# Optimization experiments

Measured on AMD Instinct MI355X. Metric: run time of the kernel, lower is better.

## Reference

```python
import jax, jax.numpy as jnp
import numpy as np

B, S, D, H = 2, 2048, 1024, 16
DK = D // H


def setup_inputs() -> dict:
    key = jax.random.key(0)
    ks = jax.random.split(key, 12)
    s = 0.02
    inp = {
        "query": jax.random.normal(ks[0], (B, S, D), jnp.float32),
        "key": jax.random.normal(ks[1], (B, S, D), jnp.float32),
        "value": jax.random.normal(ks[2], (B, S, D), jnp.float32),
        # causal mask, broadcast over heads inside reference
        "mask": jnp.broadcast_to(jnp.tril(jnp.ones((S, S), jnp.int32)), (B, S, S)),
        "Wq": jax.random.normal(ks[3], (D, D), jnp.float32) * s,
        "bq": jnp.zeros((D,), jnp.float32),
        "Wk": jax.random.normal(ks[4], (D, D), jnp.float32) * s,
        "bk": jnp.zeros((D,), jnp.float32),
        "Wv": jax.random.normal(ks[5], (D, D), jnp.float32) * s,
        "bv": jnp.zeros((D,), jnp.float32),
        "Wo": jax.random.normal(ks[6], (D, D), jnp.float32) * s,
        "bo": jnp.zeros((D,), jnp.float32),
    }
    return inp


def reference(query, key, value, mask, Wq, bq, Wk, bk, Wv, bv, Wo, bo):
    b, sq, d = query.shape
    sk = key.shape[1]
    # projections (torch Linear: x @ W.T + b)
    q = (jnp.einsum('bsd,ed->bse', query, Wq) + bq).reshape(b, sq, H, DK).transpose(0, 2, 1, 3)
    k = (jnp.einsum('bsd,ed->bse', key, Wk) + bk).reshape(b, sk, H, DK).transpose(0, 2, 1, 3)
    v = (jnp.einsum('bsd,ed->bse', value, Wv) + bv).reshape(b, sk, H, DK).transpose(0, 2, 1, 3)
    # scaled dot-product attention, full score matrix as in the original
    scores = jnp.einsum('bhqd,bhkd->bhqk', q, k) / jnp.sqrt(jnp.float32(DK))
    scores = jnp.where(mask[:, None, :, :] == 0, jnp.float32(-1e9), scores)
    p_attn = jax.nn.softmax(scores, axis=-1)  # dropout omitted (eval mode)
    x = jnp.einsum('bhqk,bhkd->bhqd', p_attn, v)
    x = x.transpose(0, 2, 1, 3).reshape(b, sq, d)
    return jnp.einsum('bsd,ed->bse', x, Wo) + bo
```

## Files before the change

### kernel.cpp

```cpp
#include <hip/hip_runtime.h>
#include <hip/hip_bf16.h>

typedef __attribute__((ext_vector_type(8))) short short8;
typedef __attribute__((ext_vector_type(4))) short short4v;
typedef __attribute__((ext_vector_type(4))) float f32x4;

__device__ __forceinline__ short f2bf(float x) {
    __hip_bfloat16 h = __float2bfloat16(x);
    return __builtin_bit_cast(short, h);
}

__device__ __forceinline__ float exp2v(float x) {
    float r;
    asm("v_exp_f32 %0, %1" : "=v"(r) : "v"(x));
    return r;
}

__device__ __forceinline__ void gload16(const void* g, void* l) {
    __builtin_amdgcn_global_load_lds(
        (const __attribute__((address_space(1))) void*)g,
        (__attribute__((address_space(3))) void*)l, 16, 0, 0);
}

__global__ __launch_bounds__(256) void cvt_all_kernel(
    const float* __restrict__ q, const float* __restrict__ k,
    const float* __restrict__ v, const float* __restrict__ wq,
    const float* __restrict__ wk, const float* __restrict__ wv,
    const float* __restrict__ wo, short* __restrict__ dst) {
    size_t i = ((size_t)blockIdx.x * 256 + threadIdx.x) * 8;
    const float* s; size_t si;
    if (i < 12582912) {
        int w = (int)(i >> 22);
        s = (w == 0) ? q : (w == 1) ? k : v;
        si = i & 4194303;
    } else {
        size_t j = i - 12582912;
        int w = (int)(j >> 20);
        s = (w == 0) ? wq : (w == 1) ? wk : (w == 2) ? wv : wo;
        si = j & 1048575;
    }
    float4 a = *(const float4*)(s + si);
    float4 b = *(const float4*)(s + si + 4);
    short8 o;
    o[0] = f2bf(a.x); o[1] = f2bf(a.y); o[2] = f2bf(a.z); o[3] = f2bf(a.w);
    o[4] = f2bf(b.x); o[5] = f2bf(b.y); o[6] = f2bf(b.z); o[7] = f2bf(b.w);
    *(short8*)(dst + i) = o;
}

__device__ __forceinline__ void gemm128_core(const char* Ab, const char* Wb,
                                             short* Al, short* Bl,
                                             f32x4 (&acc)[4][4]) {
    const int tid = threadIdx.x, lane = tid & 63, wid = tid >> 6;
    const int lr = lane & 15, lg = lane >> 4;
    const int wr = wid >> 1, wc = wid & 1;
    for (int kt = 0; kt < 32; ++kt) {
#pragma unroll
        for (int i = 0; i < 2; ++i) {
            int slot0 = (wid * 2 + i) * 64;
            int slot = slot0 + lane;
            int row = slot >> 2;
            int cb = (slot & 3) << 4;
            size_t goff = (size_t)row * 2048 + (kt << 6) + cb;
            gload16(Ab + goff, (char*)Al + (slot0 << 4));
            gload16(Wb + goff, (char*)Bl + (slot0 << 4));
        }
        __syncthreads();
        short8 af[4], bw[4];
#pragma unroll
        for (int m = 0; m < 4; ++m)
            af[m] = *(const short8*)(Al + ((64 * wr + 16 * m + lr) << 5) + (lg << 3));
#pragma unroll
        for (int n = 0; n < 4; ++n)
            bw[n] = *(const short8*)(Bl + ((64 * wc + 16 * n + lr) << 5) + (lg << 3));
#pragma unroll
        for (int m = 0; m < 4; ++m)
#pragma unroll
            for (int n = 0; n < 4; ++n)
                acc[m][n] = __builtin_amdgcn_mfma_f32_16x16x32_bf16(
                    af[m], bw[n], acc[m][n], 0, 0, 0);
        __syncthreads();
    }
}

__global__ __launch_bounds__(256) void proj_gemm_kernel(
    const __hip_bfloat16* __restrict__ ins,
    const __hip_bfloat16* __restrict__ wts,
    const float* __restrict__ b0, const float* __restrict__ b1,
    const float* __restrict__ b2,
    __hip_bfloat16* __restrict__ outs) {
    __shared__ __align__(16) short Sh[2][128 * 32];
    const int lin = blockIdx.x;
    const int logical = ((lin & 7) * 96) + (lin >> 3);
    const int bx = logical & 7;
    const int by = (logical >> 3) & 31;
    const int z  = logical >> 8;
    const char* Ab = (const char*)(ins + (size_t)z * 4194304)
                     + (size_t)by * 128 * 2048;
    const char* Wb = (const char*)(wts + (size_t)z * 1048576)
                     + (size_t)bx * 128 * 2048;
    const float* bias = (z == 0) ? b0 : (z == 1) ? b1 : b2;
    __hip_bfloat16* out = outs + (size_t)z * 4194304;

    f32x4 acc[4][4] = {};
    gemm128_core(Ab, Wb, Sh[0], Sh[1], acc);

    const int tid = threadIdx.x, lane = tid & 63, wid = tid >> 6;
    const int lr = lane & 15, lg = lane >> 4;
    const int wr = wid >> 1, wc = wid & 1;
    int col0 = (bx << 7) + (wc << 6);
    int row0 = (by << 7) + (wr << 6);

    if (z == 2) {
        char* tb = (char*)Sh;
#pragma unroll
        for (int hm = 0; hm < 2; ++hm) {
            if (wr == hm) {
#pragma unroll
                for (int n = 0; n < 4; ++n) {
                    int coll = (wc << 6) + 16 * n + lr;
                    float bb = bias[(bx << 7) + coll];
#pragma unroll
                    for (int m = 0; m < 4; ++m) {
                        short4v vv;
#pragma unroll
                        for (int r = 0; r < 4; ++r)
                            vv[r] = f2bf(acc[m][n][r] + bb);
                        int byteoff = coll * 128 + 32 * m + 8 * lg;
                        *(short4v*)(tb + (byteoff ^ ((coll & 7) << 4))) = vv;
                    }
                }
            }
            __syncthreads();
#pragma unroll
            for (int i = 0; i < 4; ++i) {
                int c = tid + (i << 8);
                int row = c >> 3;
                int pos = c & 7;
                int lb = row * 128 + (pos << 4);
                short8 vv = *(const short8*)(tb + (lb ^ ((row & 7) << 4)));
                int e = (bx << 7) + row;
                int hh = e >> 6, dk = e & 63;
                int srow = (by << 7) + (hm << 6) + (pos << 3);
                int bat = srow >> 11, s = srow & 2047;
                *(short8*)((short*)out +
                    ((size_t)((bat * 16 + hh) * 64 + dk) << 11) + s) = vv;
            }
            __syncthreads();
        }
        return;
    }

    const float scale = (z == 0) ? 0.125f * 1.44269504f : 1.0f;
#pragma unroll
    for (int n = 0; n < 4; ++n) {
        int col = col0 + 16 * n + lr;
        float bb = bias[col];
        int hh = col >> 6, dk = col & 63;
#pragma unroll
        for (int m = 0; m < 4; ++m)
#pragma unroll
            for (int r = 0; r < 4; ++r) {
                int row = row0 + 16 * m + 4 * lg + r;
                int bat = row >> 11, s = row & 2047;
                out[((size_t)((bat * 16 + hh) * 2048 + s) << 6) + dk] =
                    __float2bfloat16((acc[m][n][r] + bb) * scale);
            }
    }
}

__global__ __launch_bounds__(256) void out_gemm_kernel(
    const __hip_bfloat16* __restrict__ X, const __hip_bfloat16* __restrict__ Wo,
    const float* __restrict__ bias, float* __restrict__ out) {
    __shared__ __align__(16) short Al[64 * 32];
    __shared__ __align__(16) short Bl[128 * 32];
    const int lin = blockIdx.x;
    const int logical = ((lin & 7) * 64) + (lin >> 3);
    const int bx = logical & 7;
    const int by = logical >> 3;
    const char* Ab = (const char*)X + (size_t)by * 64 * 2048;
    const char* Wb = (const char*)Wo + (size_t)bx * 128 * 2048;
    const int tid = threadIdx.x, lane = tid & 63, wid = tid >> 6;
    const int lr = lane & 15, lg = lane >> 4;

    f32x4 acc[4][2] = {};
    for (int kt = 0; kt < 32; ++kt) {
        {
            int slotA = (wid << 6) + lane;
            int rowA = slotA >> 2, cbA = (slotA & 3) << 4;
            gload16(Ab + (size_t)rowA * 2048 + (kt << 6) + cbA,
                    (char*)Al + (wid << 10));
#pragma unroll
            for (int i = 0; i < 2; ++i) {
                int slot0 = (wid * 2 + i) * 64;
                int slot = slot0 + lane;
                int rowB = slot >> 2, cbB = (slot & 3) << 4;
                gload16(Wb + (size_t)rowB * 2048 + (kt << 6) + cbB,
                        (char*)Bl + (slot0 << 4));
            }
        }
        __syncthreads();
        short8 af[4], bw[2];
#pragma unroll
        for (int m = 0; m < 4; ++m)
            af[m] = *(const short8*)(Al + ((16 * m + lr) << 5) + (lg << 3));
#pragma unroll
        for (int n = 0; n < 2; ++n)
            bw[n] = *(const short8*)(Bl + ((32 * wid + 16 * n + lr) << 5) + (lg << 3));
#pragma unroll
        for (int m = 0; m < 4; ++m)
#pragma unroll
            for (int n = 0; n < 2; ++n)
                acc[m][n] = __builtin_amdgcn_mfma_f32_16x16x32_bf16(
                    af[m], bw[n], acc[m][n], 0, 0, 0);
        __syncthreads();
    }

    int col0 = (bx << 7) + (wid << 5);
    int row0 = (by << 6);
#pragma unroll
    for (int n = 0; n < 2; ++n) {
        int col = col0 + 16 * n + lr;
        float bb = bias[col];
#pragma unroll
        for (int m = 0; m < 4; ++m)
#pragma unroll
            for (int r = 0; r < 4; ++r) {
                int row = row0 + 16 * m + 4 * lg + r;
                out[((size_t)row << 10) + col] = acc[m][n][r] + bb;
            }
    }
}

#define SWZB(row, cb) ((cb) ^ (((row) & 7) << 4))
#define RESCALE_THR 10.0f

__device__ __forceinline__ void stage_kv(const short* kg, const short* vtg,
                                         short* Kbuf, short* Vbuf, int kv0,
                                         int wid, int lane) {
#pragma unroll
    for (int i = 0; i < 2; ++i) {
        int slot0 = (wid * 2 + i) * 64;
        int slot = slot0 + lane;
        int row = slot >> 3;
        int cb = (slot & 7) << 4;
        const char* gk = (const char*)(kg + (size_t)(kv0 + row) * 64)
                         + SWZB(row, cb);
        gload16(gk, (char*)Kbuf + (slot0 << 4));
        const char* gv = (const char*)(vtg + (size_t)row * 2048 + kv0)
                         + SWZB(row, cb);
        gload16(gv, (char*)Vbuf + (slot0 << 4));
    }
}

__global__ __launch_bounds__(256) void attn_kernel(
    const __hip_bfloat16* __restrict__ qb, const __hip_bfloat16* __restrict__ kb,
    const __hip_bfloat16* __restrict__ vtb, __hip_bfloat16* __restrict__ xb) {
    __shared__ __align__(16) short Kl[2][64 * 64];
    __shared__ __align__(16) short Vl[2][64 * 64];
    __shared__ __align__(16) short Pl[4][16 * 64];
    const int tid = threadIdx.x, lane = tid & 63, wid = tid >> 6;
    const int lr = lane & 15, lg = lane >> 4;
    const int lin = blockIdx.x;
    const int logical = ((lin & 7) * 64) + (lin >> 3);
    const int px = logical & 15;
    const int h = (logical >> 4) & 15;
    const int b = logical >> 8;
    const size_t hb = (size_t)(b * 16 + h) * (2048 * 64);
    const short* qg = (const short*)qb + hb;
    const short* kg = (const short*)kb + hb;
    const short* vtg = (const short*)vtb + hb;
    char* pw = (char*)Pl[wid];
    const short8 ones = {16256, 16256, 16256, 16256,
                         16256, 16256, 16256, 16256};
    const int csrc = (lane & 48) | ((lane >> 2) & 12);

#pragma unroll 1
    for (int half = 0; half < 2; ++half) {
        const int qt = half ? (31 - px) : px;
        const int q0 = qt << 6;
        const int ntiles = qt + 1;

        short8 qa[2];
        const char* qrow = (const char*)(qg + (size_t)q0 * 64)
                           + (16 * wid + lr) * 128 + (lg << 4);
        qa[0] = *(const short8*)(qrow);
        qa[1] = *(const short8*)(qrow + 64);

        f32x4 o[4] = {};
        f32x4 lacc = {};
        float m = -1e30f;
        const int qcol = q0 + 16 * wid + lr;
        const int qorow = q0 + 16 * wid + 4 * lg;

        stage_kv(kg, vtg, Kl[0], Vl[0], 0, wid, lane);
        int cur = 0;
#pragma unroll 1
        for (int t = 0; t < ntiles; ++t) {
            if (t + 1 < ntiles) {
                stage_kv(kg, vtg, Kl[cur ^ 1], Vl[cur ^ 1], (t + 1) << 6,
                         wid, lane);
                asm volatile("s_waitcnt vmcnt(4)" ::: "memory");
            } else {
                asm volatile("s_waitcnt vmcnt(0)" ::: "memory");
            }
            __builtin_amdgcn_s_barrier();

            const char* Kc = (const char*)Kl[cur];
            const char* Vc = (const char*)Vl[cur];

            f32x4 sc[4] = {};
            __builtin_amdgcn_s_setprio(1);
#pragma unroll
            for (int kk = 0; kk < 2; ++kk)
#pragma unroll
                for (int n = 0; n < 4; ++n) {
                    int row = 16 * n + lr;
                    short8 kf = *(const short8*)(Kc + row * 128 +
                                    SWZB(row, kk * 64 + (lg << 4)));
                    sc[n] = __builtin_amdgcn_mfma_f32_16x16x32_bf16(
                        kf, qa[kk], sc[n], 0, 0, 0);
                }
            __builtin_amdgcn_s_setprio(0);

            if (t == qt) {
                const int kv0 = t << 6;
#pragma unroll
                for (int n = 0; n < 4; ++n)
#pragma unroll
                    for (int r = 0; r < 4; ++r)
                        if (kv0 + 16 * n + 4 * lg + r > qcol)
                            sc[n][r] = -1e30f;
            }

            float pm;
            {
                float t0 = fmaxf(fmaxf(sc[0][0], sc[0][1]),
                                 fmaxf(sc[0][2], sc[0][3]));
                float t1 = fmaxf(fmaxf(sc[1][0], sc[1][1]),
                                 fmaxf(sc[1][2], sc[1][3]));
                float t2 = fmaxf(fmaxf(sc[2][0], sc[2][1]),
                                 fmaxf(sc[2][2], sc[2][3]));
                float t3 = fmaxf(fmaxf(sc[3][0], sc[3][1]),
                                 fmaxf(sc[3][2], sc[3][3]));
                pm = fmaxf(fmaxf(t0, t1), fmaxf(t2, t3));
                pm = fmaxf(pm, __shfl_xor(pm, 16));
                pm = fmaxf(pm, __shfl_xor(pm, 32));
            }

            if (__any(pm > m + RESCALE_THR)) {
                float mnew = fmaxf(m, pm);
                float corrq = exp2v(m - mnew);
                m = mnew;
#pragma unroll
                for (int r = 0; r < 4; ++r) {
                    float c = __shfl(corrq, csrc + r);
                    lacc[r] *= c;
#pragma unroll
                    for (int nd = 0; nd < 4; ++nd) o[nd][r] *= c;
                }
            }

#pragma unroll
            for (int n = 0; n < 4; ++n)
#pragma unroll
                for (int rr = 0; rr < 2; ++rr) {
                    float p0 = exp2v(sc[n][2 * rr] - m);
                    float p1 = exp2v(sc[n][2 * rr + 1] - m);
                    unsigned w;
                    asm("v_cvt_pk_bf16_f32 %0, %1, %2"
                        : "=v"(w) : "v"(p0), "v"(p1));
                    int bcol = 32 * n + 8 * lg + 4 * rr;
                    *(unsigned*)(pw + lr * 128 + SWZB(lr, bcol)) = w;
                }

            __builtin_amdgcn_s_setprio(1);
#pragma unroll
            for (int kk = 0; kk < 2; ++kk) {
                short8 pa = *(const short8*)(pw + lr * 128 +
                                SWZB(lr, kk * 64 + (lg << 4)));
                lacc = __builtin_amdgcn_mfma_f32_16x16x32_bf16(
                    pa, ones, lacc, 0, 0, 0);
#pragma unroll
                for (int nd = 0; nd < 4; ++nd) {
                    int row = 16 * nd + lr;
                    short8 vf = *(const short8*)(Vc + row * 128 +
                                    SWZB(row, kk * 64 + (lg << 4)));
                    o[nd] = __builtin_amdgcn_mfma_f32_16x16x32_bf16(
                        pa, vf, o[nd], 0, 0, 0);
                }
            }
            __builtin_amdgcn_s_setprio(0);
            __builtin_amdgcn_s_barrier();
            cur ^= 1;
        }

#pragma unroll
        for (int r = 0; r < 4; ++r) {
            float inv = 1.0f / lacc[r];
            int s = qorow + r;
            size_t rowoff = ((size_t)(b * 2048 + s) << 10) + (h << 6);
#pragma unroll
            for (int nd = 0; nd < 4; ++nd)
                xb[rowoff + 16 * nd + lr] = __float2bfloat16(o[nd][r] * inv);
        }
    }
}

extern "C" void kernel_launch(void* const* d_in, const int* in_sizes, int n_in,
                              void* d_out, int out_size, void* d_ws, size_t ws_size,
                              hipStream_t stream) {
    const float* query = (const float*)d_in[0];
    const float* key_  = (const float*)d_in[1];
    const float* value = (const float*)d_in[2];
    const float* Wq = (const float*)d_in[4];
    const float* bq = (const float*)d_in[5];
    const float* Wk = (const float*)d_in[6];
    const float* bk = (const float*)d_in[7];
    const float* Wv = (const float*)d_in[8];
    const float* bv = (const float*)d_in[9];
    const float* Wo = (const float*)d_in[10];
    const float* bo = (const float*)d_in[11];

    __hip_bfloat16* ws    = (__hip_bfloat16*)d_ws;
    __hip_bfloat16* in_b  = ws;
    __hip_bfloat16* w_b   = ws + 12582912;
    __hip_bfloat16* qkv_b = ws + 16777216;
    __hip_bfloat16* x_b   = ws;

    cvt_all_kernel<<<8192, 256, 0, stream>>>(query, key_, value,
                                             Wq, Wk, Wv, Wo, (short*)in_b);
    proj_gemm_kernel<<<768, 256, 0, stream>>>(in_b, w_b, bq, bk, bv, qkv_b);
    attn_kernel<<<512, 256, 0, stream>>>(qkv_b, qkv_b + 4194304,
                                         qkv_b + 8388608, x_b);
    out_gemm_kernel<<<512, 256, 0, stream>>>(x_b, w_b + 3145728, bo,
                                             (float*)d_out);
}
```

Before: 125.9 us.

## Split KV tile across two warp groups in attention with merged softmax states

The attention kernel now runs 8 waves per block instead of 4. Each group of 4 waves handles one half of the 64-wide KV tile for the same 16-row query slices. The two partial online-softmax states (max, sum, output) are merged through shared memory at the end of each query tile, with one staging load per thread. The intent is to raise wave count and latency hiding, and to halve the per-wave serial MFMA and exp chain per tile. The cost is extra barriers, LDS traffic for the merge, and duplicated Q loads and rescale work.

```diff
diff --git a/kernel.cpp b/kernel.cpp
--- a/kernel.cpp
+++ b/kernel.cpp
@@ -234,31 +234,12 @@
 #define SWZB(row, cb) ((cb) ^ (((row) & 7) << 4))
 #define RESCALE_THR 10.0f
 
-__device__ __forceinline__ void stage_kv(const short* kg, const short* vtg,
-                                         short* Kbuf, short* Vbuf, int kv0,
-                                         int wid, int lane) {
-#pragma unroll
-    for (int i = 0; i < 2; ++i) {
-        int slot0 = (wid * 2 + i) * 64;
-        int slot = slot0 + lane;
-        int row = slot >> 3;
-        int cb = (slot & 7) << 4;
-        const char* gk = (const char*)(kg + (size_t)(kv0 + row) * 64)
-                         + SWZB(row, cb);
-        gload16(gk, (char*)Kbuf + (slot0 << 4));
-        const char* gv = (const char*)(vtg + (size_t)row * 2048 + kv0)
-                         + SWZB(row, cb);
-        gload16(gv, (char*)Vbuf + (slot0 << 4));
-    }
-}
-
-__global__ __launch_bounds__(256) void attn_kernel(
+__global__ __launch_bounds__(512) void attn_kernel(
     const __hip_bfloat16* __restrict__ qb, const __hip_bfloat16* __restrict__ kb,
     const __hip_bfloat16* __restrict__ vtb, __hip_bfloat16* __restrict__ xb) {
-    __shared__ __align__(16) short Kl[2][64 * 64];
-    __shared__ __align__(16) short Vl[2][64 * 64];
-    __shared__ __align__(16) short Pl[4][16 * 64];
+    __shared__ __align__(16) char smem[40960];
     const int tid = threadIdx.x, lane = tid & 63, wid = tid >> 6;
+    const int ws = wid & 3, kvh = wid >> 2;
     const int lr = lane & 15, lg = lane >> 4;
     const int lin = blockIdx.x;
     const int logical = ((lin & 7) * 64) + (lin >> 3);
@@ -269,10 +250,12 @@
     const short* qg = (const short*)qb + hb;
     const short* kg = (const short*)kb + hb;
     const short* vtg = (const short*)vtb + hb;
-    char* pw = (char*)Pl[wid];
+    char* pw = smem + 32768 + ws * 2048;
     const short8 ones = {16256, 16256, 16256, 16256,
                          16256, 16256, 16256, 16256};
     const int csrc = (lane & 48) | ((lane >> 2) & 12);
+    const int srow = tid >> 3, scb = (tid & 7) << 4;
+    const int sswz = SWZB(srow, scb);
 
 #pragma unroll 1
     for (int half = 0; half < 2; ++half) {
@@ -282,39 +265,47 @@
 
         short8 qa[2];
         const char* qrow = (const char*)(qg + (size_t)q0 * 64)
-                           + (16 * wid + lr) * 128 + (lg << 4);
+                           + (16 * ws + lr) * 128 + (lg << 4);
         qa[0] = *(const short8*)(qrow);
         qa[1] = *(const short8*)(qrow + 64);
 
         f32x4 o[4] = {};
         f32x4 lacc = {};
         float m = -1e30f;
-        const int qcol = q0 + 16 * wid + lr;
-        const int qorow = q0 + 16 * wid + 4 * lg;
-
-        stage_kv(kg, vtg, Kl[0], Vl[0], 0, wid, lane);
+        const int qcol = q0 + 16 * ws + lr;
+        const int qorow = q0 + 16 * ws + 4 * lg;
+
+        {
+            gload16((const char*)(kg + (size_t)srow * 64) + sswz,
+                    smem + (wid << 10));
+            gload16((const char*)(vtg + (size_t)srow * 2048) + sswz,
+                    smem + 16384 + (wid << 10));
+        }
         int cur = 0;
 #pragma unroll 1
         for (int t = 0; t < ntiles; ++t) {
             if (t + 1 < ntiles) {
-                stage_kv(kg, vtg, Kl[cur ^ 1], Vl[cur ^ 1], (t + 1) << 6,
-                         wid, lane);
-                asm volatile("s_waitcnt vmcnt(4)" ::: "memory");
+                const int kv0 = (t + 1) << 6;
+                gload16((const char*)(kg + (size_t)(kv0 + srow) * 64) + sswz,
+                        smem + ((cur ^ 1) << 13) + (wid << 10));
+                gload16((const char*)(vtg + (size_t)srow * 2048 + kv0) + sswz,
+                        smem + 16384 + ((cur ^ 1) << 13) + (wid << 10));
+                asm volatile("s_waitcnt vmcnt(2)" ::: "memory");
             } else {
                 asm volatile("s_waitcnt vmcnt(0)" ::: "memory");
             }
             __builtin_amdgcn_s_barrier();
 
-            const char* Kc = (const char*)Kl[cur];
-            const char* Vc = (const char*)Vl[cur];
-
-            f32x4 sc[4] = {};
+            const char* Kc = smem + (cur << 13);
+            const char* Vc = smem + 16384 + (cur << 13);
+
+            f32x4 sc[2] = {};
             __builtin_amdgcn_s_setprio(1);
 #pragma unroll
             for (int kk = 0; kk < 2; ++kk)
 #pragma unroll
-                for (int n = 0; n < 4; ++n) {
-                    int row = 16 * n + lr;
+                for (int n = 0; n < 2; ++n) {
+                    int row = 32 * kvh + 16 * n + lr;
                     short8 kf = *(const short8*)(Kc + row * 128 +
                                     SWZB(row, kk * 64 + (lg << 4)));
                     sc[n] = __builtin_amdgcn_mfma_f32_16x16x32_bf16(
@@ -323,12 +314,12 @@
             __builtin_amdgcn_s_setprio(0);
 
             if (t == qt) {
-                const int kv0 = t << 6;
-#pragma unroll
-                for (int n = 0; n < 4; ++n)
+                const int kvb = (t << 6) + 32 * kvh;
+#pragma unroll
+                for (int n = 0; n < 2; ++n)
 #pragma unroll
                     for (int r = 0; r < 4; ++r)
-                        if (kv0 + 16 * n + 4 * lg + r > qcol)
+                        if (kvb + 16 * n + 4 * lg + r > qcol)
                             sc[n][r] = -1e30f;
             }
 
@@ -338,11 +329,7 @@
                                  fmaxf(sc[0][2], sc[0][3]));
                 float t1 = fmaxf(fmaxf(sc[1][0], sc[1][1]),
                                  fmaxf(sc[1][2], sc[1][3]));
-                float t2 = fmaxf(fmaxf(sc[2][0], sc[2][1]),
-                                 fmaxf(sc[2][2], sc[2][3]));
-                float t3 = fmaxf(fmaxf(sc[3][0], sc[3][1]),
-                                 fmaxf(sc[3][2], sc[3][3]));
-                pm = fmaxf(fmaxf(t0, t1), fmaxf(t2, t3));
+                pm = fmaxf(t0, t1);
                 pm = fmaxf(pm, __shfl_xor(pm, 16));
                 pm = fmaxf(pm, __shfl_xor(pm, 32));
             }
@@ -361,7 +348,7 @@
             }
 
 #pragma unroll
-            for (int n = 0; n < 4; ++n)
+            for (int n = 0; n < 2; ++n)
 #pragma unroll
                 for (int rr = 0; rr < 2; ++rr) {
                     float p0 = exp2v(sc[n][2 * rr] - m);
@@ -369,22 +356,21 @@
                     unsigned w;
                     asm("v_cvt_pk_bf16_f32 %0, %1, %2"
                         : "=v"(w) : "v"(p0), "v"(p1));
-                    int bcol = 32 * n + 8 * lg + 4 * rr;
+                    int bcol = 64 * kvh + 32 * n + 8 * lg + 4 * rr;
                     *(unsigned*)(pw + lr * 128 + SWZB(lr, bcol)) = w;
                 }
 
             __builtin_amdgcn_s_setprio(1);
-#pragma unroll
-            for (int kk = 0; kk < 2; ++kk) {
+            {
                 short8 pa = *(const short8*)(pw + lr * 128 +
-                                SWZB(lr, kk * 64 + (lg << 4)));
+                                SWZB(lr, kvh * 64 + (lg << 4)));
                 lacc = __builtin_amdgcn_mfma_f32_16x16x32_bf16(
                     pa, ones, lacc, 0, 0, 0);
 #pragma unroll
                 for (int nd = 0; nd < 4; ++nd) {
                     int row = 16 * nd + lr;
                     short8 vf = *(const short8*)(Vc + row * 128 +
-                                    SWZB(row, kk * 64 + (lg << 4)));
+                                    SWZB(row, kvh * 64 + (lg << 4)));
                     o[nd] = __builtin_amdgcn_mfma_f32_16x16x32_bf16(
                         pa, vf, o[nd], 0, 0, 0);
                 }
@@ -394,15 +380,44 @@
             cur ^= 1;
         }
 
-#pragma unroll
-        for (int r = 0; r < 4; ++r) {
-            float inv = 1.0f / lacc[r];
-            int s = qorow + r;
-            size_t rowoff = ((size_t)(b * 2048 + s) << 10) + (h << 6);
+        float* mb = (float*)smem;
+        const int mi = ((ws << 6) + lane) * 25;
+        float mo[4];
+#pragma unroll
+        for (int r = 0; r < 4; ++r) mo[r] = __shfl(m, csrc + r);
+        if (kvh == 1) {
+#pragma unroll
+            for (int r = 0; r < 4; ++r) {
+                mb[mi + r] = mo[r];
+                mb[mi + 4 + r] = lacc[r];
+            }
 #pragma unroll
             for (int nd = 0; nd < 4; ++nd)
-                xb[rowoff + 16 * nd + lr] = __float2bfloat16(o[nd][r] * inv);
-        }
+#pragma unroll
+                for (int r = 0; r < 4; ++r)
+                    mb[mi + 8 + nd * 4 + r] = o[nd][r];
+        }
+        asm volatile("s_waitcnt lgkmcnt(0)" ::: "memory");
+        __builtin_amdgcn_s_barrier();
+        if (kvh == 0) {
+#pragma unroll
+            for (int r = 0; r < 4; ++r) {
+                float mB = mb[mi + r];
+                float lB = mb[mi + 4 + r];
+                float M = fmaxf(mo[r], mB);
+                float cA = exp2v(mo[r] - M);
+                float cB = exp2v(mB - M);
+                float inv = 1.0f / (lacc[r] * cA + lB * cB);
+                int s = qorow + r;
+                size_t rowoff = ((size_t)(b * 2048 + s) << 10) + (h << 6);
+#pragma unroll
+                for (int nd = 0; nd < 4; ++nd) {
+                    float ov = o[nd][r] * cA + mb[mi + 8 + nd * 4 + r] * cB;
+                    xb[rowoff + 16 * nd + lr] = __float2bfloat16(ov * inv);
+                }
+            }
+        }
+        __builtin_amdgcn_s_barrier();
     }
 }
 
@@ -430,7 +445,7 @@
     cvt_all_kernel<<<8192, 256, 0, stream>>>(query, key_, value,
                                              Wq, Wk, Wv, Wo, (short*)in_b);
     proj_gemm_kernel<<<768, 256, 0, stream>>>(in_b, w_b, bq, bk, bv, qkv_b);
-    attn_kernel<<<512, 256, 0, stream>>>(qkv_b, qkv_b + 4194304,
+    attn_kernel<<<512, 512, 0, stream>>>(qkv_b, qkv_b + 4194304,
                                          qkv_b + 8388608, x_b);
     out_gemm_kernel<<<512, 256, 0, stream>>>(x_b, w_b + 3145728, bo,
                                              (float*)d_out);
```

Measured after the change: 117.9 us. 1.07x faster.
